# Kernel tuning notes

Measured on AMD Instinct MI355X. Metric: run time of the kernel, lower is better.

## Reference

```python
import jax, jax.numpy as jnp
import numpy as np

N_ING, N_DIR = 100000, 50000
E = 1000000
H, D = 4, 16          # heads, per-head dim
HID = H * D           # 64
LAT, COND = 32, 8
F_ING, F_DIR = 16, 8
OUT_ING = 16


def _han_edge(x_src, x_dst, att_s, att_d, edge_index, n_dst):
    # HANConv per-edge-type attention message passing.
    src, dst = edge_index[0], edge_index[1]
    a = jax.nn.leaky_relu(
        jnp.einsum('nhd,hd->nh', x_src, att_s)[src]
        + jnp.einsum('nhd,hd->nh', x_dst, att_d)[dst],
        negative_slope=0.2)                               # [E, H]
    amax = jax.ops.segment_max(a, dst, num_segments=n_dst)
    ex = jnp.exp(a - amax[dst])
    denom = jax.ops.segment_sum(ex, dst, num_segments=n_dst)
    alpha = ex / (denom[dst] + 1e-16)                     # PyG softmax eps
    out = jax.ops.segment_sum(x_src[src] * alpha[:, :, None], dst,
                              num_segments=n_dst)         # [n_dst, H, D]
    return jax.nn.relu(out.reshape(n_dst, HID))


def _group(outs, q, Wk, bk):
    # HANConv semantic-level attention across edge types.
    s = jnp.stack(outs)                                   # [T, N, HID]
    score = jnp.tanh(s @ Wk + bk).mean(axis=1) @ q        # [T]
    attn = jax.nn.softmax(score)
    return jnp.einsum('t,tnf->nf', attn, s)


def setup_inputs() -> dict:
    key = jax.random.key(0)
    ks = jax.random.split(key, 32)
    def ei(k, n_src, n_dst):
        k1, k2 = jax.random.split(k)
        return jnp.stack([jax.random.randint(k1, (E,), 0, n_src),
                          jax.random.randint(k2, (E,), 0, n_dst)]).astype(jnp.int64)
    s = 0.1
    inp = {
        'x_ing': jax.random.normal(ks[0], (N_ING, F_ING), jnp.float32),
        'x_dir': jax.random.normal(ks[1], (N_DIR, F_DIR), jnp.float32),
        'cond':  jax.random.normal(ks[2], (COND,), jnp.float32),
        'eps':   jax.random.normal(ks[3], (1, LAT), jnp.float32),
        'ei_cooc':     ei(ks[4], N_ING, N_DIR),
        'ei_used':     ei(ks[5], N_ING, N_DIR),
        'ei_contains': ei(ks[6], N_DIR, N_ING),
        'ei_pairs':    ei(ks[7], N_DIR, N_DIR),
        'ei_follows':  ei(ks[8], N_DIR, N_DIR),
        # node-type projections
        'W_pi': jax.random.normal(ks[9],  (F_ING, HID)) * s,
        'b_pi': jnp.zeros((HID,)),
        'W_pd': jax.random.normal(ks[10], (F_DIR, HID)) * s,
        'b_pd': jnp.zeros((HID,)),
        # semantic attention
        'Wk': jax.random.normal(ks[21], (HID, HID)) * s,
        'bk': jnp.zeros((HID,)),
        'q':  jax.random.normal(ks[22], (HID,)) * s,
        # VAE heads (input: 2*HID + COND)
        'W_mu': jax.random.normal(ks[23], (2 * HID + COND, LAT)) * s,
        'b_mu': jnp.zeros((LAT,)),
        'W_lv': jax.random.normal(ks[24], (2 * HID + COND, LAT)) * s,
        'b_lv': jnp.zeros((LAT,)),
        # decoder (fc1 is dead code in the original forward)
        'W_fc3': jax.random.normal(ks[25], (LAT, HID)) * s,
        'b_fc3': jnp.zeros((HID,)),
        'W_fc2': jax.random.normal(ks[26], (HID, OUT_ING)) * s,
        'b_fc2': jnp.zeros((OUT_ING,)),
    }
    for i, name in enumerate(['cooc', 'used', 'contains', 'pairs', 'follows']):
        inp[f'as_{name}'] = jax.random.normal(ks[11 + i], (H, D)) * s
        inp[f'ad_{name}'] = jax.random.normal(ks[16 + i], (H, D)) * s
    return inp


def reference(x_ing, x_dir, cond, eps,
              ei_cooc, ei_used, ei_contains, ei_pairs, ei_follows,
              W_pi, b_pi, W_pd, b_pd,
              as_cooc, ad_cooc, as_used, ad_used, as_contains, ad_contains,
              as_pairs, ad_pairs, as_follows, ad_follows,
              Wk, bk, q, W_mu, b_mu, W_lv, b_lv,
              W_fc3, b_fc3, W_fc2, b_fc2):
    # node-type projections -> [N, H, D]
    h_ing = (x_ing @ W_pi + b_pi).reshape(N_ING, H, D)
    h_dir = (x_dir @ W_pd + b_pd).reshape(N_DIR, H, D)

    o_cooc = _han_edge(h_ing, h_dir, as_cooc, ad_cooc, ei_cooc, N_DIR)
    o_used = _han_edge(h_ing, h_dir, as_used, ad_used, ei_used, N_DIR)
    o_cont = _han_edge(h_dir, h_ing, as_contains, ad_contains, ei_contains, N_ING)
    o_pair = _han_edge(h_dir, h_dir, as_pairs, ad_pairs, ei_pairs, N_DIR)
    o_foll = _han_edge(h_dir, h_dir, as_follows, ad_follows, ei_follows, N_DIR)

    out_ing = _group([o_cont], q, Wk, bk)                       # [N_ING, HID]
    out_dir = _group([o_cooc, o_used, o_pair, o_foll], q, Wk, bk)

    ingre_pool = out_ing.mean(axis=0, keepdims=True)            # [1, HID]
    direc_pool = out_dir.mean(axis=0, keepdims=True)
    graph_repr = jnp.concatenate([ingre_pool, direc_pool, cond[None]], axis=1)

    mu = graph_repr @ W_mu + b_mu
    logvar = graph_repr @ W_lv + b_lv
    z = mu + eps * jnp.exp(0.5 * logvar)

    # decoder: fc1 branch is overwritten in the original; effective path below
    recon = jnp.tanh(jax.nn.relu(z @ W_fc3 + b_fc3) @ W_fc2 + b_fc2)  # [1, OUT_ING]
    return recon, mu, logvar
```

## Files before the change

### kernel.cpp

```cpp
#include <hip/hip_runtime.h>
#include <hip/hip_fp16.h>
#include <math.h>

#define N_ING 100000
#define N_DIR 50000
#define NE    1000000
#define NDST_TOTAL 300000
#define NBUCK 586
#define BSH   9
#define BMSK  511
#define BA    64
#define NBK   (5 * BA)
#define I4PT  (NE / 4)
#define PB_ING 384
#define PB_DIR 192
#define BPAIR_CAP (5 * NE + 16 * NBUCK)
#define LOG2E 1.442695041f

typedef float v2f __attribute__((ext_vector_type(2)));
typedef __attribute__((ext_vector_type(8))) short bf16x8;
typedef __attribute__((ext_vector_type(4))) float f32x4;

__global__ __launch_bounds__(1024) void k0_hist(
    const int* __restrict__ e0, const int* __restrict__ e1,
    const int* __restrict__ e2, const int* __restrict__ e3,
    const int* __restrict__ e4, int* __restrict__ blockcnt)
{
    __shared__ int hist[NBUCK];
    const int bid = blockIdx.x;
    const int tid = threadIdx.x;
    const int type = bid / BA, blk = bid % BA;
    const int* ei = type == 0 ? e0 : type == 1 ? e1 : type == 2 ? e2
                  : type == 3 ? e3 : e4;
    const int base = type == 0 ? 0 : type == 1 ? 50000 : type == 2 ? 100000
                   : type == 3 ? 200000 : 250000;
    for (int i = tid; i < NBUCK; i += 1024) hist[i] = 0;
    __syncthreads();
    const int4* d4 = (const int4*)(ei + NE);
    for (int i = blk * 1024 + tid; i < I4PT; i += BA * 1024) {
        int4 d = d4[i];
        atomicAdd(&hist[(base + d.x) >> BSH], 1);
        atomicAdd(&hist[(base + d.y) >> BSH], 1);
        atomicAdd(&hist[(base + d.z) >> BSH], 1);
        atomicAdd(&hist[(base + d.w) >> BSH], 1);
    }
    __syncthreads();
    int* row = blockcnt + (size_t)bid * NBUCK;
    for (int i = tid; i < NBUCK; i += 1024) row[i] = hist[i];
}

__global__ __launch_bounds__(256) void kA_kernel(
    const float* __restrict__ x_ing, const float* __restrict__ W_pi,
    const float* __restrict__ b_pi,
    const float* __restrict__ as_cooc, const float* __restrict__ as_used,
    const float* __restrict__ ad_contains,
    unsigned* __restrict__ h8_ing, __half* __restrict__ s_ing,
    const float* __restrict__ x_dir, const float* __restrict__ W_pd,
    const float* __restrict__ b_pd,
    const float* __restrict__ ad_cooc, const float* __restrict__ ad_used,
    const float* __restrict__ as_contains, const float* __restrict__ as_pairs,
    const float* __restrict__ ad_pairs, const float* __restrict__ as_follows,
    const float* __restrict__ ad_follows,
    unsigned* __restrict__ h8_dir, __half* __restrict__ s_dir)
{
    __shared__ float sW[16 * 64];
    __shared__ float sbb[64];
    __shared__ float satt[7 * 64];
    __shared__ float sx[4][16];
    __shared__ float srow[4][64];

    const int bid = blockIdx.x;
    const int tid = threadIdx.x;
    if (bid < PB_ING) {
        const int g = tid >> 6, t = tid & 63;
        for (int i = tid; i < 16 * 64; i += 256) sW[i] = W_pi[i];
        if (tid < 64) {
            sbb[tid] = b_pi[tid];
            satt[tid]       = as_cooc[tid] * LOG2E;
            satt[64 + tid]  = as_used[tid] * LOG2E;
            satt[128 + tid] = ad_contains[tid] * LOG2E;
        }
        __syncthreads();
        for (int q = bid; q < N_ING / 4; q += PB_ING) {
            int n = q * 4 + g;
            if (t < 16) sx[g][t] = x_ing[(size_t)n * 16 + t];
            __syncthreads();
            float s = sbb[t];
#pragma unroll
            for (int i = 0; i < 16; ++i) s += sx[g][i] * sW[i * 64 + t];
            srow[g][t] = s;
            __syncthreads();
            if (t < 16) {
                int w0 = __builtin_amdgcn_cvt_pk_fp8_f32(srow[g][t * 4], srow[g][t * 4 + 1], 0, false);
                int w  = __builtin_amdgcn_cvt_pk_fp8_f32(srow[g][t * 4 + 2], srow[g][t * 4 + 3], w0, true);
                h8_ing[(size_t)n * 16 + t] = (unsigned)w;
            }
            if (t < 12) {
                int slot = t >> 2, hh = t & 3;
                float sc = 0.f;
#pragma unroll
                for (int d = 0; d < 16; ++d)
                    sc += srow[g][hh * 16 + d] * satt[slot * 64 + hh * 16 + d];
                s_ing[(size_t)n * 12 + t] = __float2half(sc);
            }
            __syncthreads();
        }
    } else {
        const int g = tid >> 6, t = tid & 63;
        for (int i = tid; i < 8 * 64; i += 256) sW[i] = W_pd[i];
        if (tid < 64) {
            sbb[tid] = b_pd[tid];
            satt[tid]        = ad_cooc[tid] * LOG2E;
            satt[64  + tid]  = ad_used[tid] * LOG2E;
            satt[128 + tid]  = as_contains[tid] * LOG2E;
            satt[192 + tid]  = as_pairs[tid] * LOG2E;
            satt[256 + tid]  = ad_pairs[tid] * LOG2E;
            satt[320 + tid]  = as_follows[tid] * LOG2E;
            satt[384 + tid]  = ad_follows[tid] * LOG2E;
        }
        __syncthreads();
        for (int q = bid - PB_ING; q < N_DIR / 4; q += PB_DIR) {
            int n = q * 4 + g;
            if (t < 8) sx[g][t] = x_dir[(size_t)n * 8 + t];
            __syncthreads();
            float s = sbb[t];
#pragma unroll
            for (int i = 0; i < 8; ++i) s += sx[g][i] * sW[i * 64 + t];
            srow[g][t] = s;
            __syncthreads();
            if (t < 16) {
                int w0 = __builtin_amdgcn_cvt_pk_fp8_f32(srow[g][t * 4], srow[g][t * 4 + 1], 0, false);
                int w  = __builtin_amdgcn_cvt_pk_fp8_f32(srow[g][t * 4 + 2], srow[g][t * 4 + 3], w0, true);
                h8_dir[(size_t)n * 16 + t] = (unsigned)w;
            }
            if (t < 28) {
                int slot = t >> 2, hh = t & 3;
                float sc = 0.f;
#pragma unroll
                for (int d = 0; d < 16; ++d)
                    sc += srow[g][hh * 16 + d] * satt[slot * 64 + hh * 16 + d];
                s_dir[(size_t)n * 28 + t] = __float2half(sc);
            }
            __syncthreads();
        }
    }
}

__global__ __launch_bounds__(256) void k2_kernel(
    const int* __restrict__ blockcnt, int* __restrict__ blockbase,
    int* __restrict__ bbase, int* __restrict__ btot, int* __restrict__ cursor)
{
    __shared__ int part[4][64];
    __shared__ int tots[64];
    __shared__ int scn[64];
    __shared__ int bw;
    const int tid = threadIdx.x;
    const int kq = tid >> 6, bl = tid & 63;
    const int b = blockIdx.x * 64 + bl;
    const int K = NBK / 4;
    int ps = 0;
    if (b < NBUCK)
        for (int k = kq * K; k < kq * K + K; ++k)
            ps += blockcnt[(size_t)k * NBUCK + b];
    part[kq][bl] = ps;
    __syncthreads();
    if (tid < 64) {
        int t = part[0][tid] + part[1][tid] + part[2][tid] + part[3][tid];
        tots[tid] = t;
        scn[tid] = (t + 15) & ~15;
    }
    __syncthreads();
    for (int off = 1; off < 64; off <<= 1) {
        int v = 0;
        if (tid < 64 && tid >= off) v = scn[tid - off];
        __syncthreads();
        if (tid < 64) scn[tid] += v;
        __syncthreads();
    }
    if (tid == 63) bw = atomicAdd(cursor, scn[63]);
    __syncthreads();
    if (b < NBUCK) {
        int pad = (tots[bl] + 15) & ~15;
        int bs = bw + scn[bl] - pad;
        if (kq == 0) {
            bbase[b] = bs;
            btot[b] = tots[bl];
        }
        int run = bs;
        for (int q = 0; q < kq; ++q) run += part[q][bl];
        for (int k = kq * K; k < kq * K + K; ++k) {
            blockbase[(size_t)k * NBUCK + b] = run;
            run += blockcnt[(size_t)k * NBUCK + b];
        }
    }
}

__global__ __launch_bounds__(1024) void k3_kernel(
    const int* __restrict__ e0, const int* __restrict__ e1,
    const int* __restrict__ e2, const int* __restrict__ e3,
    const int* __restrict__ e4, const int* __restrict__ blockbase,
    unsigned* __restrict__ bpair)
{
    __shared__ int cur[NBUCK];
    const int bid = blockIdx.x, tid = threadIdx.x;
    const int type = bid / BA, blk = bid % BA;
    const int* ei = type == 0 ? e0 : type == 1 ? e1 : type == 2 ? e2
                  : type == 3 ? e3 : e4;
    const int base = type == 0 ? 0 : type == 1 ? 50000 : type == 2 ? 100000
                   : type == 3 ? 200000 : 250000;
    const int* row = blockbase + (size_t)bid * NBUCK;
    for (int i = tid; i < NBUCK; i += 1024) cur[i] = row[i];
    __syncthreads();
    const int4* s4 = (const int4*)ei;
    const int4* d4 = (const int4*)(ei + NE);
    for (int i = blk * 1024 + tid; i < I4PT; i += BA * 1024) {
        int4 s = s4[i];
        int4 d = d4[i];
        int g0 = base + d.x, g1 = base + d.y, g2 = base + d.z, g3 = base + d.w;
        int p0 = atomicAdd(&cur[g0 >> BSH], 1);
        int p1 = atomicAdd(&cur[g1 >> BSH], 1);
        int p2 = atomicAdd(&cur[g2 >> BSH], 1);
        int p3 = atomicAdd(&cur[g3 >> BSH], 1);
        bpair[p0] = ((unsigned)(g0 & BMSK) << 17) | (unsigned)s.x;
        bpair[p1] = ((unsigned)(g1 & BMSK) << 17) | (unsigned)s.y;
        bpair[p2] = ((unsigned)(g2 & BMSK) << 17) | (unsigned)s.z;
        bpair[p3] = ((unsigned)(g3 & BMSK) << 17) | (unsigned)s.w;
    }
}

__global__ __launch_bounds__(512) void k4_kernel(
    const unsigned* __restrict__ bpair, const int* __restrict__ bbase,
    const int* __restrict__ btot, int* __restrict__ perm,
    int* __restrict__ start, int* __restrict__ cnt)
{
    __shared__ int h[512], cu[512], sc[512];
    const int b = blockIdx.x, tid = threadIdx.x;
    const int jb = bbase[b], n = btot[b];
    h[tid] = 0;
    __syncthreads();
    for (int i = tid; i < n; i += 512)
        atomicAdd(&h[bpair[jb + i] >> 17], 1);
    __syncthreads();
    int v = h[tid];
    sc[tid] = v;
    __syncthreads();
    for (int off = 1; off < 512; off <<= 1) {
        int t2 = 0;
        if (tid >= off) t2 = sc[tid - off];
        __syncthreads();
        sc[tid] += t2;
        __syncthreads();
    }
    int ex = sc[tid] - v;
    cu[tid] = ex;
    int dg = b * 512 + tid;
    if (dg < NDST_TOTAL) { start[dg] = jb + ex; cnt[dg] = v; }
    __syncthreads();
    for (int i = tid; i < n; i += 512) {
        unsigned p = bpair[jb + i];
        int pos = atomicAdd(&cu[p >> 17], 1);
        perm[jb + pos] = (int)(p & 0x1FFFF);
    }
}

__global__ __launch_bounds__(256) void agg_all_kernel(
    const int* __restrict__ perm, const int* __restrict__ start,
    const int* __restrict__ cnttot,
    const unsigned* __restrict__ h8_ing, const unsigned* __restrict__ h8_dir,
    const __half* __restrict__ s_ing, const __half* __restrict__ s_dir,
    unsigned* __restrict__ rows8,
    float* __restrict__ pool_ing, float* __restrict__ pool_dir)
{
    __shared__ __align__(16) float srow[4][64];
    __shared__ float sred[4][64];
    const int t = threadIdx.x & 63, w = threadIdx.x >> 6;
    const int g  = t >> 4;
    const int l4 = t & 15;
    const int hq = l4 >> 2;

    float p_ing = 0.f;
    float p0 = 0.f, p1 = 0.f, p2 = 0.f, p3 = 0.f;
    const int nwaves = gridDim.x * 4;
    for (int d = blockIdx.x * 4 + w; d < NDST_TOTAL; d += nwaves) {
        int type, ld;
        const __half *ssrc, *sdst;
        const unsigned* hsrc;
        unsigned uss, uds; int soff, doff;
        if (d < 50000)       { type = 0; ld = d;          ssrc = s_ing; uss = 12; soff = 0;  sdst = s_dir; uds = 28; doff = 0;  hsrc = h8_ing; }
        else if (d < 100000) { type = 1; ld = d - 50000;  ssrc = s_ing; uss = 12; soff = 4;  sdst = s_dir; uds = 28; doff = 4;  hsrc = h8_ing; }
        else if (d < 200000) { type = 2; ld = d - 100000; ssrc = s_dir; uss = 28; soff = 8;  sdst = s_ing; uds = 12; doff = 8;  hsrc = h8_dir; }
        else if (d < 250000) { type = 3; ld = d - 200000; ssrc = s_dir; uss = 28; soff = 12; sdst = s_dir; uds = 28; doff = 16; hsrc = h8_dir; }
        else                 { type = 4; ld = d - 250000; ssrc = s_dir; uss = 28; soff = 20; sdst = s_dir; uds = 28; doff = 24; hsrc = h8_dir; }
        float adst = __half2float(sdst[(unsigned)ld * uds + (unsigned)(doff + hq)]);
        const unsigned usoff = (unsigned)(soff + hq);
        int jb = start[d], je = jb + cnttot[d];
        int jl = je - 1;
        float4 acc = make_float4(0.f, 0.f, 0.f, 0.f);
        float dsum = 0.f;
        for (int j = jb; j < je; j += 16) {
            int j0 = j + g, j1 = j + 4 + g, j2 = j + 8 + g, j3 = j + 12 + g;
            bool v0 = j0 < je, v1 = j1 < je, v2 = j2 < je, v3 = j3 < je;
            unsigned s0 = (unsigned)perm[v0 ? j0 : jl];
            unsigned s1 = (unsigned)perm[v1 ? j1 : jl];
            unsigned s2 = (unsigned)perm[v2 ? j2 : jl];
            unsigned s3 = (unsigned)perm[v3 ? j3 : jl];
            float c0 = __half2float(ssrc[s0 * uss + usoff]);
            float c1 = __half2float(ssrc[s1 * uss + usoff]);
            float c2 = __half2float(ssrc[s2 * uss + usoff]);
            float c3 = __half2float(ssrc[s3 * uss + usoff]);
            unsigned u0 = hsrc[s0 * 16u + (unsigned)l4];
            unsigned u1 = hsrc[s1 * 16u + (unsigned)l4];
            unsigned u2 = hsrc[s2 * 16u + (unsigned)l4];
            unsigned u3 = hsrc[s3 * 16u + (unsigned)l4];
            float a0 = c0 + adst; a0 = a0 > 0.f ? a0 : 0.2f * a0;
            float a1 = c1 + adst; a1 = a1 > 0.f ? a1 : 0.2f * a1;
            float a2 = c2 + adst; a2 = a2 > 0.f ? a2 : 0.2f * a2;
            float a3 = c3 + adst; a3 = a3 > 0.f ? a3 : 0.2f * a3;
            float e0 = v0 ? __builtin_amdgcn_exp2f(a0) : 0.f;
            float e1 = v1 ? __builtin_amdgcn_exp2f(a1) : 0.f;
            float e2 = v2 ? __builtin_amdgcn_exp2f(a2) : 0.f;
            float e3 = v3 ? __builtin_amdgcn_exp2f(a3) : 0.f;
            dsum += (e0 + e1) + (e2 + e3);
            v2f lo0 = __builtin_amdgcn_cvt_pk_f32_fp8((int)u0, false);
            v2f hi0 = __builtin_amdgcn_cvt_pk_f32_fp8((int)u0, true);
            v2f lo1 = __builtin_amdgcn_cvt_pk_f32_fp8((int)u1, false);
            v2f hi1 = __builtin_amdgcn_cvt_pk_f32_fp8((int)u1, true);
            v2f lo2 = __builtin_amdgcn_cvt_pk_f32_fp8((int)u2, false);
            v2f hi2 = __builtin_amdgcn_cvt_pk_f32_fp8((int)u2, true);
            v2f lo3 = __builtin_amdgcn_cvt_pk_f32_fp8((int)u3, false);
            v2f hi3 = __builtin_amdgcn_cvt_pk_f32_fp8((int)u3, true);
            acc.x += (lo0.x * e0 + lo1.x * e1) + (lo2.x * e2 + lo3.x * e3);
            acc.y += (lo0.y * e0 + lo1.y * e1) + (lo2.y * e2 + lo3.y * e3);
            acc.z += (hi0.x * e0 + hi1.x * e1) + (hi2.x * e2 + hi3.x * e3);
            acc.w += (hi0.y * e0 + hi1.y * e1) + (hi2.y * e2 + hi3.y * e3);
        }
#pragma unroll
        for (int mask = 16; mask <= 32; mask <<= 1) {
            acc.x += __shfl_xor(acc.x, mask, 64);
            acc.y += __shfl_xor(acc.y, mask, 64);
            acc.z += __shfl_xor(acc.z, mask, 64);
            acc.w += __shfl_xor(acc.w, mask, 64);
            dsum  += __shfl_xor(dsum,  mask, 64);
        }
        float inv = 1.f / (dsum + 1e-16f);
        float4 v4 = make_float4(fmaxf(acc.x * inv, 0.f), fmaxf(acc.y * inv, 0.f),
                                fmaxf(acc.z * inv, 0.f), fmaxf(acc.w * inv, 0.f));
        if (g == 0) *(float4*)&srow[w][l4 * 4] = v4;
        float v = srow[w][t];
        if (type == 2) {
            p_ing += v;
        } else {
            if (type == 0)      p0 += v;
            else if (type == 1) p1 += v;
            else if (type == 3) p2 += v;
            else                p3 += v;
            if (g == 0) {
                unsigned md = (unsigned)(d < 100000 ? d : d - 100000);
                int r0 = __builtin_amdgcn_cvt_pk_fp8_f32(v4.x, v4.y, 0, false);
                int r1 = __builtin_amdgcn_cvt_pk_fp8_f32(v4.z, v4.w, r0, true);
                rows8[md * 16u + (unsigned)l4] = (unsigned)r1;
            }
        }
    }
    float vals[5] = { p_ing, p0, p1, p2, p3 };
    float* outs[5] = { pool_ing, pool_dir, pool_dir + 64, pool_dir + 128,
                       pool_dir + 192 };
    for (int i = 0; i < 5; ++i) {
        __syncthreads();
        sred[w][t] = vals[i];
        __syncthreads();
        if (w == 0)
            atomicAdd(&outs[i][t], sred[0][t] + sred[1][t] + sred[2][t] + sred[3][t]);
    }
}

__global__ __launch_bounds__(256) void sem_kernel(
    const unsigned* __restrict__ rows8, const float* __restrict__ Wk,
    const float* __restrict__ bk, float* __restrict__ sem_dir)
{
    __shared__ float swk[4096];
    __shared__ float ssem[256];
    const int tid = threadIdx.x;
    for (int i = tid; i < 4096; i += 256) swk[i] = Wk[i];
    ssem[tid] = 0.f;
    __syncthreads();

    const int lane = tid & 63, w = tid >> 6;
    const int col = lane & 15, kg = lane >> 4;

    bf16x8 bfr[4][2];
    float biasv[4];
#pragma unroll
    for (int nt = 0; nt < 4; ++nt) {
        biasv[nt] = bk[nt * 16 + col];
#pragma unroll
        for (int ks = 0; ks < 2; ++ks) {
            bf16x8 bb;
#pragma unroll
            for (int j = 0; j < 8; ++j) {
                int k = ks * 32 + kg * 8 + j;
                unsigned u = __builtin_bit_cast(unsigned, swk[k * 64 + nt * 16 + col]);
                u = u + 0x7FFFu + ((u >> 16) & 1u);
                bb[j] = (short)(u >> 16);
            }
            bfr[nt][ks] = bb;
        }
    }

    const int gw = blockIdx.x * 4 + w;
    const int nw = gridDim.x * 4;
    for (int tile = gw; tile < 12500; tile += nw) {
        const int tt = tile / 3125;
        const unsigned* rp = rows8 + (unsigned)(tile * 16 + col) * 16u;
        bf16x8 afr[2];
#pragma unroll
        for (int ks = 0; ks < 2; ++ks) {
            uint2 uu = *(const uint2*)(rp + ks * 8 + kg * 2);
            v2f l0 = __builtin_amdgcn_cvt_pk_f32_fp8((int)uu.x, false);
            v2f h0 = __builtin_amdgcn_cvt_pk_f32_fp8((int)uu.x, true);
            v2f l1 = __builtin_amdgcn_cvt_pk_f32_fp8((int)uu.y, false);
            v2f h1 = __builtin_amdgcn_cvt_pk_f32_fp8((int)uu.y, true);
            bf16x8 aa;
            aa[0] = (short)(__builtin_bit_cast(unsigned, l0.x) >> 16);
            aa[1] = (short)(__builtin_bit_cast(unsigned, l0.y) >> 16);
            aa[2] = (short)(__builtin_bit_cast(unsigned, h0.x) >> 16);
            aa[3] = (short)(__builtin_bit_cast(unsigned, h0.y) >> 16);
            aa[4] = (short)(__builtin_bit_cast(unsigned, l1.x) >> 16);
            aa[5] = (short)(__builtin_bit_cast(unsigned, l1.y) >> 16);
            aa[6] = (short)(__builtin_bit_cast(unsigned, h1.x) >> 16);
            aa[7] = (short)(__builtin_bit_cast(unsigned, h1.y) >> 16);
            afr[ks] = aa;
        }
#pragma unroll
        for (int nt = 0; nt < 4; ++nt) {
            f32x4 acc = {0.f, 0.f, 0.f, 0.f};
            acc = __builtin_amdgcn_mfma_f32_16x16x32_bf16(afr[0], bfr[nt][0], acc, 0, 0, 0);
            acc = __builtin_amdgcn_mfma_f32_16x16x32_bf16(afr[1], bfr[nt][1], acc, 0, 0, 0);
            float s = 0.f;
#pragma unroll
            for (int reg = 0; reg < 4; ++reg) {
                float x = acc[reg] + biasv[nt];
                x = fminf(fmaxf(x, -15.f), 15.f);
                float e = __builtin_amdgcn_exp2f(x * (2.f * LOG2E));
                s += (e - 1.f) * __builtin_amdgcn_rcpf(e + 1.f);
            }
            s += __shfl_xor(s, 16, 64);
            s += __shfl_xor(s, 32, 64);
            if (lane < 16) atomicAdd(&ssem[tt * 64 + nt * 16 + col], s);
        }
    }
    __syncthreads();
    atomicAdd(&sem_dir[tid], ssem[tid]);
}

__global__ __launch_bounds__(64) void final_kernel(
    const float* __restrict__ pool_ing, const float* __restrict__ pool_dir,
    const float* __restrict__ sem_dir, const float* __restrict__ q,
    const float* __restrict__ cond, const float* __restrict__ eps,
    const float* __restrict__ W_mu, const float* __restrict__ b_mu,
    const float* __restrict__ W_lv, const float* __restrict__ b_lv,
    const float* __restrict__ W_fc3, const float* __restrict__ b_fc3,
    const float* __restrict__ W_fc2, const float* __restrict__ b_fc2,
    float* __restrict__ out)
{
    __shared__ float gr[136];
    __shared__ float sc[4], attn[4];
    __shared__ float z[32], hfc[64];
    int t = threadIdx.x;
    if (t < 4) {
        float s = 0.f;
        for (int f = 0; f < 64; ++f)
            s += (sem_dir[t * 64 + f] / (float)N_DIR) * q[f];
        sc[t] = s;
    }
    gr[t] = pool_ing[t] / (float)N_ING;
    __syncthreads();
    if (t == 0) {
        float m = fmaxf(fmaxf(sc[0], sc[1]), fmaxf(sc[2], sc[3]));
        float ssum = 0.f;
        for (int i = 0; i < 4; ++i) { attn[i] = expf(sc[i] - m); ssum += attn[i]; }
        for (int i = 0; i < 4; ++i) attn[i] /= ssum;
    }
    __syncthreads();
    {
        float v = 0.f;
        for (int tt = 0; tt < 4; ++tt)
            v += attn[tt] * (pool_dir[tt * 64 + t] / (float)N_DIR);
        gr[64 + t] = v;
    }
    if (t < 8) gr[128 + t] = cond[t];
    __syncthreads();
    if (t < 32) {
        float m = b_mu[t], lv = b_lv[t];
        for (int i = 0; i < 136; ++i) {
            float g = gr[i];
            m  += g * W_mu[i * 32 + t];
            lv += g * W_lv[i * 32 + t];
        }
        out[16 + t] = m;
        out[48 + t] = lv;
        z[t] = m + eps[t] * expf(0.5f * lv);
    }
    __syncthreads();
    {
        float v = b_fc3[t];
        for (int j = 0; j < 32; ++j) v += z[j] * W_fc3[j * 64 + t];
        hfc[t] = fmaxf(v, 0.f);
    }
    __syncthreads();
    if (t < 16) {
        float v = b_fc2[t];
        for (int f = 0; f < 64; ++f) v += hfc[f] * W_fc2[f * 16 + t];
        out[t] = tanhf(v);
    }
}

extern "C" void kernel_launch(void* const* d_in, const int* in_sizes, int n_in,
                              void* d_out, int out_size, void* d_ws, size_t ws_size,
                              hipStream_t stream) {
    const float* x_ing = (const float*)d_in[0];
    const float* x_dir = (const float*)d_in[1];
    const float* cond  = (const float*)d_in[2];
    const float* eps   = (const float*)d_in[3];
    const int* ei_cooc     = (const int*)d_in[4];
    const int* ei_used     = (const int*)d_in[5];
    const int* ei_contains = (const int*)d_in[6];
    const int* ei_pairs    = (const int*)d_in[7];
    const int* ei_follows  = (const int*)d_in[8];
    const float* W_pi = (const float*)d_in[9];
    const float* b_pi = (const float*)d_in[10];
    const float* W_pd = (const float*)d_in[11];
    const float* b_pd = (const float*)d_in[12];
    const float* Wk   = (const float*)d_in[13];
    const float* bk   = (const float*)d_in[14];
    const float* q    = (const float*)d_in[15];
    const float* W_mu = (const float*)d_in[16];
    const float* b_mu = (const float*)d_in[17];
    const float* W_lv = (const float*)d_in[18];
    const float* b_lv = (const float*)d_in[19];
    const float* W_fc3 = (const float*)d_in[20];
    const float* b_fc3 = (const float*)d_in[21];
    const float* W_fc2 = (const float*)d_in[22];
    const float* b_fc2 = (const float*)d_in[23];
    const float* as_cooc     = (const float*)d_in[24];
    const float* ad_cooc     = (const float*)d_in[25];
    const float* as_used     = (const float*)d_in[26];
    const float* ad_used     = (const float*)d_in[27];
    const float* as_contains = (const float*)d_in[28];
    const float* ad_contains = (const float*)d_in[29];
    const float* as_pairs    = (const float*)d_in[30];
    const float* ad_pairs    = (const float*)d_in[31];
    const float* as_follows  = (const float*)d_in[32];
    const float* ad_follows  = (const float*)d_in[33];

    unsigned* bpair = (unsigned*)d_ws;
    unsigned* h8_ing = bpair + (size_t)BPAIR_CAP;
    unsigned* h8_dir = h8_ing + (size_t)N_ING * 16;
    __half* s_ing = (__half*)(h8_dir + (size_t)N_DIR * 16);
    __half* s_dir = s_ing + (size_t)N_ING * 12;
    int*   perm  = (int*)(s_dir + (size_t)N_DIR * 28);
    int*   bbase  = perm + (size_t)BPAIR_CAP;
    int*   btot   = bbase + NBUCK;
    int*   start  = btot + NBUCK;
    int*   cnt    = start + NDST_TOTAL;
    int*   cursor = cnt + NDST_TOTAL;
    float* pool_ing = (float*)(cursor + 1);
    float* pool_dir = pool_ing + 64;
    float* sem_dir  = pool_dir + 256;
    unsigned* rows8 = bpair;
    int* blockcnt  = (int*)bpair;
    int* blockbase = (int*)perm;

    hipMemsetAsync(cursor, 0, (1 + 64 + 256 + 256) * sizeof(int), stream);

    k0_hist<<<NBK, 1024, 0, stream>>>(
        ei_cooc, ei_used, ei_contains, ei_pairs, ei_follows, blockcnt);

    kA_kernel<<<PB_ING + PB_DIR, 256, 0, stream>>>(
        x_ing, W_pi, b_pi, as_cooc, as_used, ad_contains, h8_ing, s_ing,
        x_dir, W_pd, b_pd, ad_cooc, ad_used, as_contains, as_pairs, ad_pairs,
        as_follows, ad_follows, h8_dir, s_dir);

    k2_kernel<<<(NBUCK + 63) / 64, 256, 0, stream>>>(
        blockcnt, blockbase, bbase, btot, cursor);

    k3_kernel<<<NBK, 1024, 0, stream>>>(
        ei_cooc, ei_used, ei_contains, ei_pairs, ei_follows, blockbase, bpair);

    k4_kernel<<<NBUCK, 512, 0, stream>>>(bpair, bbase, btot, perm, start, cnt);

    agg_all_kernel<<<2048, 256, 0, stream>>>(
        perm, start, cnt, h8_ing, h8_dir, s_ing, s_dir, rows8,
        pool_ing, pool_dir);

    sem_kernel<<<512, 256, 0, stream>>>(rows8, Wk, bk, sem_dir);

    final_kernel<<<1, 64, 0, stream>>>(
        pool_ing, pool_dir, sem_dir, q, cond, eps,
        W_mu, b_mu, W_lv, b_lv, W_fc3, b_fc3, W_fc2, b_fc2, (float*)d_out);
}
```

Baseline: 493.7 us.

## Locally sort scatter chunks in shared memory before writing bucketed edge pairs

The bucket scatter kernel now stages each 4096-edge chunk in LDS. It builds a local histogram over the type's buckets, prefix-sums it, and reorders the chunk by bucket so the global writes to bpair land in contiguous runs instead of random 4-byte stores. The histogram and scatter kernels also switch to contiguous per-block edge ranges (80 blocks per type, 256 threads), so the order of the block counts still matches. This trades extra LDS passes and many barriers for better-coalesced global writes. It relies on each type spanning at most 256 buckets, which fits in a byte, and on I4B dividing evenly.

```diff
diff --git a/kernel.cpp b/kernel.cpp
--- a/kernel.cpp
+++ b/kernel.cpp
@@ -9,9 +9,11 @@
 #define NBUCK 586
 #define BSH   9
 #define BMSK  511
-#define BA    64
+#define BA    80
 #define NBK   (5 * BA)
 #define I4PT  (NE / 4)
+#define I4B   (I4PT / BA)
+#define CHK   1024
 #define PB_ING 384
 #define PB_DIR 192
 #define BPAIR_CAP (5 * NE + 16 * NBUCK)
@@ -21,7 +23,15 @@
 typedef __attribute__((ext_vector_type(8))) short bf16x8;
 typedef __attribute__((ext_vector_type(4))) float f32x4;
 
-__global__ __launch_bounds__(1024) void k0_hist(
+__device__ __forceinline__ void type_params(int type, const int*& ei, int& base,
+    const int* e0, const int* e1, const int* e2, const int* e3, const int* e4)
+{
+    ei = type == 0 ? e0 : type == 1 ? e1 : type == 2 ? e2 : type == 3 ? e3 : e4;
+    base = type == 0 ? 0 : type == 1 ? 50000 : type == 2 ? 100000
+         : type == 3 ? 200000 : 250000;
+}
+
+__global__ __launch_bounds__(256) void k0_hist(
     const int* __restrict__ e0, const int* __restrict__ e1,
     const int* __restrict__ e2, const int* __restrict__ e3,
     const int* __restrict__ e4, int* __restrict__ blockcnt)
@@ -30,14 +40,13 @@
     const int bid = blockIdx.x;
     const int tid = threadIdx.x;
     const int type = bid / BA, blk = bid % BA;
-    const int* ei = type == 0 ? e0 : type == 1 ? e1 : type == 2 ? e2
-                  : type == 3 ? e3 : e4;
-    const int base = type == 0 ? 0 : type == 1 ? 50000 : type == 2 ? 100000
-                   : type == 3 ? 200000 : 250000;
-    for (int i = tid; i < NBUCK; i += 1024) hist[i] = 0;
+    const int* ei; int base;
+    type_params(type, ei, base, e0, e1, e2, e3, e4);
+    for (int i = tid; i < NBUCK; i += 256) hist[i] = 0;
     __syncthreads();
     const int4* d4 = (const int4*)(ei + NE);
-    for (int i = blk * 1024 + tid; i < I4PT; i += BA * 1024) {
+    const int i0 = blk * I4B;
+    for (int i = i0 + tid; i < i0 + I4B; i += 256) {
         int4 d = d4[i];
         atomicAdd(&hist[(base + d.x) >> BSH], 1);
         atomicAdd(&hist[(base + d.y) >> BSH], 1);
@@ -46,7 +55,7 @@
     }
     __syncthreads();
     int* row = blockcnt + (size_t)bid * NBUCK;
-    for (int i = tid; i < NBUCK; i += 1024) row[i] = hist[i];
+    for (int i = tid; i < NBUCK; i += 256) row[i] = hist[i];
 }
 
 __global__ __launch_bounds__(256) void kA_kernel(
@@ -195,36 +204,85 @@
     }
 }
 
-__global__ __launch_bounds__(1024) void k3_kernel(
+__global__ __launch_bounds__(256) void k3_kernel(
     const int* __restrict__ e0, const int* __restrict__ e1,
     const int* __restrict__ e2, const int* __restrict__ e3,
     const int* __restrict__ e4, const int* __restrict__ blockbase,
     unsigned* __restrict__ bpair)
 {
-    __shared__ int cur[NBUCK];
+    __shared__ unsigned A[4 * CHK];
+    __shared__ unsigned B[4 * CHK];
+    __shared__ unsigned char LB[4 * CHK];
+    __shared__ unsigned char LB2[4 * CHK];
+    __shared__ int h[256], sc[256], cu[256], gc[256];
     const int bid = blockIdx.x, tid = threadIdx.x;
     const int type = bid / BA, blk = bid % BA;
-    const int* ei = type == 0 ? e0 : type == 1 ? e1 : type == 2 ? e2
-                  : type == 3 ? e3 : e4;
-    const int base = type == 0 ? 0 : type == 1 ? 50000 : type == 2 ? 100000
-                   : type == 3 ? 200000 : 250000;
+    const int* ei; int base;
+    type_params(type, ei, base, e0, e1, e2, e3, e4);
+    const int width = type == 2 ? 100000 : 50000;
+    const int boff = base >> BSH;
+    const int bcnt = ((base + width - 1) >> BSH) - boff + 1;
+
     const int* row = blockbase + (size_t)bid * NBUCK;
-    for (int i = tid; i < NBUCK; i += 1024) cur[i] = row[i];
-    __syncthreads();
+    for (int i = tid; i < 256; i += 256) gc[i] = (i < bcnt) ? row[boff + i] : 0;
     const int4* s4 = (const int4*)ei;
     const int4* d4 = (const int4*)(ei + NE);
-    for (int i = blk * 1024 + tid; i < I4PT; i += BA * 1024) {
-        int4 s = s4[i];
-        int4 d = d4[i];
-        int g0 = base + d.x, g1 = base + d.y, g2 = base + d.z, g3 = base + d.w;
-        int p0 = atomicAdd(&cur[g0 >> BSH], 1);
-        int p1 = atomicAdd(&cur[g1 >> BSH], 1);
-        int p2 = atomicAdd(&cur[g2 >> BSH], 1);
-        int p3 = atomicAdd(&cur[g3 >> BSH], 1);
-        bpair[p0] = ((unsigned)(g0 & BMSK) << 17) | (unsigned)s.x;
-        bpair[p1] = ((unsigned)(g1 & BMSK) << 17) | (unsigned)s.y;
-        bpair[p2] = ((unsigned)(g2 & BMSK) << 17) | (unsigned)s.z;
-        bpair[p3] = ((unsigned)(g3 & BMSK) << 17) | (unsigned)s.w;
+    const int i0 = blk * I4B;
+
+    for (int c = 0; c < I4B; c += CHK) {
+        const int nq = min(CHK, I4B - c);
+        const int n = nq * 4;
+        h[tid] = 0;
+        __syncthreads();
+        for (int q = tid; q < nq; q += 256) {
+            int4 s = s4[i0 + c + q];
+            int4 d = d4[i0 + c + q];
+            int g0 = base + d.x, g1 = base + d.y;
+            int g2 = base + d.z, g3 = base + d.w;
+            int l0 = (g0 >> BSH) - boff, l1 = (g1 >> BSH) - boff;
+            int l2 = (g2 >> BSH) - boff, l3 = (g3 >> BSH) - boff;
+            A[q * 4 + 0] = ((unsigned)(g0 & BMSK) << 17) | (unsigned)s.x;
+            A[q * 4 + 1] = ((unsigned)(g1 & BMSK) << 17) | (unsigned)s.y;
+            A[q * 4 + 2] = ((unsigned)(g2 & BMSK) << 17) | (unsigned)s.z;
+            A[q * 4 + 3] = ((unsigned)(g3 & BMSK) << 17) | (unsigned)s.w;
+            LB[q * 4 + 0] = (unsigned char)l0;
+            LB[q * 4 + 1] = (unsigned char)l1;
+            LB[q * 4 + 2] = (unsigned char)l2;
+            LB[q * 4 + 3] = (unsigned char)l3;
+            atomicAdd(&h[l0], 1);
+            atomicAdd(&h[l1], 1);
+            atomicAdd(&h[l2], 1);
+            atomicAdd(&h[l3], 1);
+        }
+        __syncthreads();
+        int v = h[tid];
+        sc[tid] = v;
+        __syncthreads();
+        for (int off = 1; off < 256; off <<= 1) {
+            int t2 = (tid >= off) ? sc[tid - off] : 0;
+            __syncthreads();
+            sc[tid] += t2;
+            __syncthreads();
+        }
+        int ex = sc[tid] - v;
+        __syncthreads();
+        sc[tid] = ex;
+        cu[tid] = ex;
+        __syncthreads();
+        for (int i = tid; i < n; i += 256) {
+            int lb = LB[i];
+            int pos = atomicAdd(&cu[lb], 1);
+            B[pos] = A[i];
+            LB2[pos] = (unsigned char)lb;
+        }
+        __syncthreads();
+        for (int j = tid; j < n; j += 256) {
+            int lb = LB2[j];
+            bpair[gc[lb] + (j - sc[lb])] = B[j];
+        }
+        __syncthreads();
+        gc[tid] += h[tid];
+        __syncthreads();
     }
 }
 
@@ -573,7 +631,7 @@
 
     hipMemsetAsync(cursor, 0, (1 + 64 + 256 + 256) * sizeof(int), stream);
 
-    k0_hist<<<NBK, 1024, 0, stream>>>(
+    k0_hist<<<NBK, 256, 0, stream>>>(
         ei_cooc, ei_used, ei_contains, ei_pairs, ei_follows, blockcnt);
 
     kA_kernel<<<PB_ING + PB_DIR, 256, 0, stream>>>(
@@ -584,7 +642,7 @@
     k2_kernel<<<(NBUCK + 63) / 64, 256, 0, stream>>>(
         blockcnt, blockbase, bbase, btot, cursor);
 
-    k3_kernel<<<NBK, 1024, 0, stream>>>(
+    k3_kernel<<<NBK, 256, 0, stream>>>(
         ei_cooc, ei_used, ei_contains, ei_pairs, ei_follows, blockbase, bpair);
 
     k4_kernel<<<NBUCK, 512, 0, stream>>>(bpair, bbase, btot, perm, start, cnt);
```

After: 494.6 us. No clear change (+0.2%).

## Fuse node projection kernel into edge scatter kernel and use contiguous edge chunks

Applied to the files above, without the earlier changes.

The node projection/score kernel is merged into the edge bucket-scatter kernel as extra blocks of one launch, so both run concurrently and one launch is removed. The histogram and scatter kernels drop from 1024 to 256 threads per block and go from 64 to 80 blocks per edge type. Each block now handles one contiguous chunk of edges instead of a grid-strided range. The k2 scan also moves ahead of the fused launch. In exchange, the shared-memory footprint of the fused kernel is the union of both, and more blockcnt rows must be scanned.

```diff
diff --git a/kernel.cpp b/kernel.cpp
--- a/kernel.cpp
+++ b/kernel.cpp
@@ -9,9 +9,10 @@
 #define NBUCK 586
 #define BSH   9
 #define BMSK  511
-#define BA    64
+#define BA    80
 #define NBK   (5 * BA)
 #define I4PT  (NE / 4)
+#define I4B   (I4PT / BA)
 #define PB_ING 384
 #define PB_DIR 192
 #define BPAIR_CAP (5 * NE + 16 * NBUCK)
@@ -21,7 +22,15 @@
 typedef __attribute__((ext_vector_type(8))) short bf16x8;
 typedef __attribute__((ext_vector_type(4))) float f32x4;
 
-__global__ __launch_bounds__(1024) void k0_hist(
+__device__ __forceinline__ void type_params(int type, const int*& ei, int& base,
+    const int* e0, const int* e1, const int* e2, const int* e3, const int* e4)
+{
+    ei = type == 0 ? e0 : type == 1 ? e1 : type == 2 ? e2 : type == 3 ? e3 : e4;
+    base = type == 0 ? 0 : type == 1 ? 50000 : type == 2 ? 100000
+         : type == 3 ? 200000 : 250000;
+}
+
+__global__ __launch_bounds__(256) void k0_hist(
     const int* __restrict__ e0, const int* __restrict__ e1,
     const int* __restrict__ e2, const int* __restrict__ e3,
     const int* __restrict__ e4, int* __restrict__ blockcnt)
@@ -30,14 +39,13 @@
     const int bid = blockIdx.x;
     const int tid = threadIdx.x;
     const int type = bid / BA, blk = bid % BA;
-    const int* ei = type == 0 ? e0 : type == 1 ? e1 : type == 2 ? e2
-                  : type == 3 ? e3 : e4;
-    const int base = type == 0 ? 0 : type == 1 ? 50000 : type == 2 ? 100000
-                   : type == 3 ? 200000 : 250000;
-    for (int i = tid; i < NBUCK; i += 1024) hist[i] = 0;
+    const int* ei; int base;
+    type_params(type, ei, base, e0, e1, e2, e3, e4);
+    for (int i = tid; i < NBUCK; i += 256) hist[i] = 0;
     __syncthreads();
     const int4* d4 = (const int4*)(ei + NE);
-    for (int i = blk * 1024 + tid; i < I4PT; i += BA * 1024) {
+    const int i0 = blk * I4B;
+    for (int i = i0 + tid; i < i0 + I4B; i += 256) {
         int4 d = d4[i];
         atomicAdd(&hist[(base + d.x) >> BSH], 1);
         atomicAdd(&hist[(base + d.y) >> BSH], 1);
@@ -46,104 +54,7 @@
     }
     __syncthreads();
     int* row = blockcnt + (size_t)bid * NBUCK;
-    for (int i = tid; i < NBUCK; i += 1024) row[i] = hist[i];
-}
-
-__global__ __launch_bounds__(256) void kA_kernel(
-    const float* __restrict__ x_ing, const float* __restrict__ W_pi,
-    const float* __restrict__ b_pi,
-    const float* __restrict__ as_cooc, const float* __restrict__ as_used,
-    const float* __restrict__ ad_contains,
-    unsigned* __restrict__ h8_ing, __half* __restrict__ s_ing,
-    const float* __restrict__ x_dir, const float* __restrict__ W_pd,
-    const float* __restrict__ b_pd,
-    const float* __restrict__ ad_cooc, const float* __restrict__ ad_used,
-    const float* __restrict__ as_contains, const float* __restrict__ as_pairs,
-    const float* __restrict__ ad_pairs, const float* __restrict__ as_follows,
-    const float* __restrict__ ad_follows,
-    unsigned* __restrict__ h8_dir, __half* __restrict__ s_dir)
-{
-    __shared__ float sW[16 * 64];
-    __shared__ float sbb[64];
-    __shared__ float satt[7 * 64];
-    __shared__ float sx[4][16];
-    __shared__ float srow[4][64];
-
-    const int bid = blockIdx.x;
-    const int tid = threadIdx.x;
-    if (bid < PB_ING) {
-        const int g = tid >> 6, t = tid & 63;
-        for (int i = tid; i < 16 * 64; i += 256) sW[i] = W_pi[i];
-        if (tid < 64) {
-            sbb[tid] = b_pi[tid];
-            satt[tid]       = as_cooc[tid] * LOG2E;
-            satt[64 + tid]  = as_used[tid] * LOG2E;
-            satt[128 + tid] = ad_contains[tid] * LOG2E;
-        }
-        __syncthreads();
-        for (int q = bid; q < N_ING / 4; q += PB_ING) {
-            int n = q * 4 + g;
-            if (t < 16) sx[g][t] = x_ing[(size_t)n * 16 + t];
-            __syncthreads();
-            float s = sbb[t];
-#pragma unroll
-            for (int i = 0; i < 16; ++i) s += sx[g][i] * sW[i * 64 + t];
-            srow[g][t] = s;
-            __syncthreads();
-            if (t < 16) {
-                int w0 = __builtin_amdgcn_cvt_pk_fp8_f32(srow[g][t * 4], srow[g][t * 4 + 1], 0, false);
-                int w  = __builtin_amdgcn_cvt_pk_fp8_f32(srow[g][t * 4 + 2], srow[g][t * 4 + 3], w0, true);
-                h8_ing[(size_t)n * 16 + t] = (unsigned)w;
-            }
-            if (t < 12) {
-                int slot = t >> 2, hh = t & 3;
-                float sc = 0.f;
-#pragma unroll
-                for (int d = 0; d < 16; ++d)
-                    sc += srow[g][hh * 16 + d] * satt[slot * 64 + hh * 16 + d];
-                s_ing[(size_t)n * 12 + t] = __float2half(sc);
-            }
-            __syncthreads();
-        }
-    } else {
-        const int g = tid >> 6, t = tid & 63;
-        for (int i = tid; i < 8 * 64; i += 256) sW[i] = W_pd[i];
-        if (tid < 64) {
-            sbb[tid] = b_pd[tid];
-            satt[tid]        = ad_cooc[tid] * LOG2E;
-            satt[64  + tid]  = ad_used[tid] * LOG2E;
-            satt[128 + tid]  = as_contains[tid] * LOG2E;
-            satt[192 + tid]  = as_pairs[tid] * LOG2E;
-            satt[256 + tid]  = ad_pairs[tid] * LOG2E;
-            satt[320 + tid]  = as_follows[tid] * LOG2E;
-            satt[384 + tid]  = ad_follows[tid] * LOG2E;
-        }
-        __syncthreads();
-        for (int q = bid - PB_ING; q < N_DIR / 4; q += PB_DIR) {
-            int n = q * 4 + g;
-            if (t < 8) sx[g][t] = x_dir[(size_t)n * 8 + t];
-            __syncthreads();
-            float s = sbb[t];
-#pragma unroll
-            for (int i = 0; i < 8; ++i) s += sx[g][i] * sW[i * 64 + t];
-            srow[g][t] = s;
-            __syncthreads();
-            if (t < 16) {
-                int w0 = __builtin_amdgcn_cvt_pk_fp8_f32(srow[g][t * 4], srow[g][t * 4 + 1], 0, false);
-                int w  = __builtin_amdgcn_cvt_pk_fp8_f32(srow[g][t * 4 + 2], srow[g][t * 4 + 3], w0, true);
-                h8_dir[(size_t)n * 16 + t] = (unsigned)w;
-            }
-            if (t < 28) {
-                int slot = t >> 2, hh = t & 3;
-                float sc = 0.f;
-#pragma unroll
-                for (int d = 0; d < 16; ++d)
-                    sc += srow[g][hh * 16 + d] * satt[slot * 64 + hh * 16 + d];
-                s_dir[(size_t)n * 28 + t] = __float2half(sc);
-            }
-            __syncthreads();
-        }
-    }
+    for (int i = tid; i < NBUCK; i += 256) row[i] = hist[i];
 }
 
 __global__ __launch_bounds__(256) void k2_kernel(
@@ -195,36 +106,129 @@
     }
 }
 
-__global__ __launch_bounds__(1024) void k3_kernel(
+__global__ __launch_bounds__(256) void k3kA_kernel(
     const int* __restrict__ e0, const int* __restrict__ e1,
     const int* __restrict__ e2, const int* __restrict__ e3,
     const int* __restrict__ e4, const int* __restrict__ blockbase,
-    unsigned* __restrict__ bpair)
+    unsigned* __restrict__ bpair,
+    const float* __restrict__ x_ing, const float* __restrict__ W_pi,
+    const float* __restrict__ b_pi,
+    const float* __restrict__ as_cooc, const float* __restrict__ as_used,
+    const float* __restrict__ ad_contains,
+    unsigned* __restrict__ h8_ing, __half* __restrict__ s_ing,
+    const float* __restrict__ x_dir, const float* __restrict__ W_pd,
+    const float* __restrict__ b_pd,
+    const float* __restrict__ ad_cooc, const float* __restrict__ ad_used,
+    const float* __restrict__ as_contains, const float* __restrict__ as_pairs,
+    const float* __restrict__ ad_pairs, const float* __restrict__ as_follows,
+    const float* __restrict__ ad_follows,
+    unsigned* __restrict__ h8_dir, __half* __restrict__ s_dir)
 {
     __shared__ int cur[NBUCK];
-    const int bid = blockIdx.x, tid = threadIdx.x;
-    const int type = bid / BA, blk = bid % BA;
-    const int* ei = type == 0 ? e0 : type == 1 ? e1 : type == 2 ? e2
-                  : type == 3 ? e3 : e4;
-    const int base = type == 0 ? 0 : type == 1 ? 50000 : type == 2 ? 100000
-                   : type == 3 ? 200000 : 250000;
-    const int* row = blockbase + (size_t)bid * NBUCK;
-    for (int i = tid; i < NBUCK; i += 1024) cur[i] = row[i];
-    __syncthreads();
-    const int4* s4 = (const int4*)ei;
-    const int4* d4 = (const int4*)(ei + NE);
-    for (int i = blk * 1024 + tid; i < I4PT; i += BA * 1024) {
-        int4 s = s4[i];
-        int4 d = d4[i];
-        int g0 = base + d.x, g1 = base + d.y, g2 = base + d.z, g3 = base + d.w;
-        int p0 = atomicAdd(&cur[g0 >> BSH], 1);
-        int p1 = atomicAdd(&cur[g1 >> BSH], 1);
-        int p2 = atomicAdd(&cur[g2 >> BSH], 1);
-        int p3 = atomicAdd(&cur[g3 >> BSH], 1);
-        bpair[p0] = ((unsigned)(g0 & BMSK) << 17) | (unsigned)s.x;
-        bpair[p1] = ((unsigned)(g1 & BMSK) << 17) | (unsigned)s.y;
-        bpair[p2] = ((unsigned)(g2 & BMSK) << 17) | (unsigned)s.z;
-        bpair[p3] = ((unsigned)(g3 & BMSK) << 17) | (unsigned)s.w;
+    __shared__ float sW[16 * 64];
+    __shared__ float sbb[64];
+    __shared__ float satt[7 * 64];
+    __shared__ float sx[4][16];
+    __shared__ float srow[4][64];
+
+    const int bid = blockIdx.x;
+    const int tid = threadIdx.x;
+    if (bid < NBK) {
+        const int type = bid / BA, blk = bid % BA;
+        const int* ei; int base;
+        type_params(type, ei, base, e0, e1, e2, e3, e4);
+        const int* row = blockbase + (size_t)bid * NBUCK;
+        for (int i = tid; i < NBUCK; i += 256) cur[i] = row[i];
+        __syncthreads();
+        const int4* s4 = (const int4*)ei;
+        const int4* d4 = (const int4*)(ei + NE);
+        const int i0 = blk * I4B;
+        for (int i = i0 + tid; i < i0 + I4B; i += 256) {
+            int4 s = s4[i];
+            int4 d = d4[i];
+            int g0 = base + d.x, g1 = base + d.y;
+            int g2 = base + d.z, g3 = base + d.w;
+            int p0 = atomicAdd(&cur[g0 >> BSH], 1);
+            int p1 = atomicAdd(&cur[g1 >> BSH], 1);
+            int p2 = atomicAdd(&cur[g2 >> BSH], 1);
+            int p3 = atomicAdd(&cur[g3 >> BSH], 1);
+            bpair[p0] = ((unsigned)(g0 & BMSK) << 17) | (unsigned)s.x;
+            bpair[p1] = ((unsigned)(g1 & BMSK) << 17) | (unsigned)s.y;
+            bpair[p2] = ((unsigned)(g2 & BMSK) << 17) | (unsigned)s.z;
+            bpair[p3] = ((unsigned)(g3 & BMSK) << 17) | (unsigned)s.w;
+        }
+    } else if (bid < NBK + PB_ING) {
+        const int g = tid >> 6, t = tid & 63;
+        for (int i = tid; i < 16 * 64; i += 256) sW[i] = W_pi[i];
+        if (tid < 64) {
+            sbb[tid] = b_pi[tid];
+            satt[tid]       = as_cooc[tid] * LOG2E;
+            satt[64 + tid]  = as_used[tid] * LOG2E;
+            satt[128 + tid] = ad_contains[tid] * LOG2E;
+        }
+        __syncthreads();
+        for (int q = bid - NBK; q < N_ING / 4; q += PB_ING) {
+            int n = q * 4 + g;
+            if (t < 16) sx[g][t] = x_ing[(size_t)n * 16 + t];
+            __syncthreads();
+            float s = sbb[t];
+#pragma unroll
+            for (int i = 0; i < 16; ++i) s += sx[g][i] * sW[i * 64 + t];
+            srow[g][t] = s;
+            __syncthreads();
+            if (t < 16) {
+                int w0 = __builtin_amdgcn_cvt_pk_fp8_f32(srow[g][t * 4], srow[g][t * 4 + 1], 0, false);
+                int w  = __builtin_amdgcn_cvt_pk_fp8_f32(srow[g][t * 4 + 2], srow[g][t * 4 + 3], w0, true);
+                h8_ing[(size_t)n * 16 + t] = (unsigned)w;
+            }
+            if (t < 12) {
+                int slot = t >> 2, hh = t & 3;
+                float sc = 0.f;
+#pragma unroll
+                for (int d = 0; d < 16; ++d)
+                    sc += srow[g][hh * 16 + d] * satt[slot * 64 + hh * 16 + d];
+                s_ing[(size_t)n * 12 + t] = __float2half(sc);
+            }
+            __syncthreads();
+        }
+    } else {
+        const int g = tid >> 6, t = tid & 63;
+        for (int i = tid; i < 8 * 64; i += 256) sW[i] = W_pd[i];
+        if (tid < 64) {
+            sbb[tid] = b_pd[tid];
+            satt[tid]        = ad_cooc[tid] * LOG2E;
+            satt[64  + tid]  = ad_used[tid] * LOG2E;
+            satt[128 + tid]  = as_contains[tid] * LOG2E;
+            satt[192 + tid]  = as_pairs[tid] * LOG2E;
+            satt[256 + tid]  = ad_pairs[tid] * LOG2E;
+            satt[320 + tid]  = as_follows[tid] * LOG2E;
+            satt[384 + tid]  = ad_follows[tid] * LOG2E;
+        }
+        __syncthreads();
+        for (int q = bid - NBK - PB_ING; q < N_DIR / 4; q += PB_DIR) {
+            int n = q * 4 + g;
+            if (t < 8) sx[g][t] = x_dir[(size_t)n * 8 + t];
+            __syncthreads();
+            float s = sbb[t];
+#pragma unroll
+            for (int i = 0; i < 8; ++i) s += sx[g][i] * sW[i * 64 + t];
+            srow[g][t] = s;
+            __syncthreads();
+            if (t < 16) {
+                int w0 = __builtin_amdgcn_cvt_pk_fp8_f32(srow[g][t * 4], srow[g][t * 4 + 1], 0, false);
+                int w  = __builtin_amdgcn_cvt_pk_fp8_f32(srow[g][t * 4 + 2], srow[g][t * 4 + 3], w0, true);
+                h8_dir[(size_t)n * 16 + t] = (unsigned)w;
+            }
+            if (t < 28) {
+                int slot = t >> 2, hh = t & 3;
+                float sc = 0.f;
+#pragma unroll
+                for (int d = 0; d < 16; ++d)
+                    sc += srow[g][hh * 16 + d] * satt[slot * 64 + hh * 16 + d];
+                s_dir[(size_t)n * 28 + t] = __float2half(sc);
+            }
+            __syncthreads();
+        }
     }
 }
 
@@ -573,20 +577,18 @@
 
     hipMemsetAsync(cursor, 0, (1 + 64 + 256 + 256) * sizeof(int), stream);
 
-    k0_hist<<<NBK, 1024, 0, stream>>>(
+    k0_hist<<<NBK, 256, 0, stream>>>(
         ei_cooc, ei_used, ei_contains, ei_pairs, ei_follows, blockcnt);
 
-    kA_kernel<<<PB_ING + PB_DIR, 256, 0, stream>>>(
+    k2_kernel<<<(NBUCK + 63) / 64, 256, 0, stream>>>(
+        blockcnt, blockbase, bbase, btot, cursor);
+
+    k3kA_kernel<<<NBK + PB_ING + PB_DIR, 256, 0, stream>>>(
+        ei_cooc, ei_used, ei_contains, ei_pairs, ei_follows, blockbase, bpair,
         x_ing, W_pi, b_pi, as_cooc, as_used, ad_contains, h8_ing, s_ing,
         x_dir, W_pd, b_pd, ad_cooc, ad_used, as_contains, as_pairs, ad_pairs,
         as_follows, ad_follows, h8_dir, s_dir);
 
-    k2_kernel<<<(NBUCK + 63) / 64, 256, 0, stream>>>(
-        blockcnt, blockbase, bbase, btot, cursor);
-
-    k3_kernel<<<NBK, 1024, 0, stream>>>(
-        ei_cooc, ei_used, ei_contains, ei_pairs, ei_follows, blockbase, bpair);
-
     k4_kernel<<<NBUCK, 512, 0, stream>>>(bpair, bbase, btot, perm, start, cnt);
 
     agg_all_kernel<<<2048, 256, 0, stream>>>(
```

Result: faster. 481.2 us (-2.5%).
